# Performance work log

Measured on AMD Instinct MI355X. Metric: run time of the kernel, lower is better.

The kernel has to match this reference:

```python
import jax, jax.numpy as jnp
import numpy as np

# module hyperparams (match init_kwargs)
C, K, S, RATIO, GC = 64, 7, 2, 2, 16
G = C // GC                      # 4 groups
KK = K * K                       # 49
NS = int(RATIO * S)              # 4
NN = NS * NS                     # 16
PAD = (K - 1) // 2               # 3
C1_IN = G * (2 * K * GC + KK)    # 1092
C1_OUT = G * NN * KK // 10       # 313
C2_OUT = G * NN * KK             # 3136
EPS = 1e-5


def _unfold(x, k, s, p):
    # torch.nn.Unfold: patches ordered (C, ki, kj) channel-major
    B, Cc, H, W = x.shape
    xp = jnp.pad(x, ((0, 0), (0, 0), (p, p), (p, p)))
    Ho = (H + 2 * p - k) // s + 1
    Wo = (W + 2 * p - k) // s + 1
    rows = jnp.arange(Ho)[:, None] * s + jnp.arange(k)[None, :]      # (Ho,k)
    cols = jnp.arange(Wo)[:, None] * s + jnp.arange(k)[None, :]      # (Wo,k)
    pat = xp[:, :, rows[:, :, None, None], cols[None, None, :, :]]   # (B,C,Ho,k,Wo,k)
    return pat.transpose(0, 1, 3, 5, 2, 4)                            # (B,C,k,k,Ho,Wo)


def setup_inputs() -> dict:
    key = jax.random.key(0)
    ks = jax.random.split(key, 5)
    x = jax.random.normal(ks[0], (8, C, 64, 64), dtype=jnp.float32)
    w1 = jax.random.normal(ks[1], (C1_OUT, C1_IN), dtype=jnp.float32) * 0.02
    gamma = jnp.ones((C1_OUT,), dtype=jnp.float32)   # BN weight (constant_init 1)
    beta = jnp.zeros((C1_OUT,), dtype=jnp.float32)   # BN bias
    w2 = jax.random.normal(ks[2], (C2_OUT, C1_OUT), dtype=jnp.float32) * 0.02
    b2 = jnp.zeros((C2_OUT,), dtype=jnp.float32)
    return {"x": x, "w1": w1, "gamma": gamma, "beta": beta, "w2": w2, "b2": b2}


def reference(x, w1, gamma, beta, w2, b2):
    B, _, H, W = x.shape
    pat = _unfold(x, K, S, PAD)                          # (B,C,K,K,Ho,Wo)
    Ho, Wo = pat.shape[-2], pat.shape[-1]
    xg = pat.reshape(B, G, GC, K, K, Ho, Wo)
    # three axis-wise max pools -> per-pixel descriptor
    x1 = xg.max(axis=2).reshape(B, G * K * K, Ho, Wo)
    x2 = xg.max(axis=3).reshape(B, G * GC * K, Ho, Wo)
    x3 = xg.max(axis=4).reshape(B, G * GC * K, Ho, Wo)
    feat = jnp.concatenate([x1, x2, x3], axis=1)         # (B, C1_IN, Ho, Wo)
    # conv1: 1x1 conv (no bias) + BN (batch stats) + ReLU
    h = jnp.einsum('bchw,oc->bohw', feat, w1)
    mu = h.mean(axis=(0, 2, 3), keepdims=True)
    var = h.var(axis=(0, 2, 3), keepdims=True)
    h = gamma[None, :, None, None] * (h - mu) * jax.lax.rsqrt(var + EPS) + beta[None, :, None, None]
    h = jax.nn.relu(h)
    # conv2: 1x1 conv with bias
    h2 = jnp.einsum('bchw,oc->bohw', h, w2) + b2[None, :, None, None]
    wt = h2.reshape(B, G, KK, NN, Ho, Wo)
    wt = jax.nn.softmax(wt, axis=2)                      # softmax over kernel positions
    # softmax-weighted patch reduction (mean over k*k)
    xk = xg.reshape(B, G, GC, KK, Ho, Wo)
    out = jnp.einsum('bgckhw,bgknhw->bgcnhw', xk, wt) / KK
    out = out.reshape(B, C, NS, NS, Ho, Wo)
    out = out.transpose(0, 1, 4, 2, 5, 3).reshape(B, C, Ho * NS, Wo * NS)
    return out
```

## Files before the change

### kernel.cpp

```cpp
#include <hip/hip_runtime.h>

namespace {
constexpr int kB    = 8;
constexpr int kC    = 64;
constexpr int kH    = 64, kW = 64;
constexpr int kNP   = 8192;
constexpr int kC1In = 1092;
constexpr int kKP   = 1152;
constexpr int kC1Out= 313;
constexpr int kC2Out= 3136;
constexpr int kC1P  = 320;
constexpr int kRowS = 56;
constexpr int kPosS = 16 * kRowS + 8;
}

typedef __attribute__((ext_vector_type(8))) short bf16x8;
typedef __attribute__((ext_vector_type(8))) _Float16 f16x8;
typedef __attribute__((ext_vector_type(2))) _Float16 h16x2;
typedef __attribute__((ext_vector_type(4))) float f32x4;

__device__ __forceinline__ unsigned short f2bf(float f) {
    unsigned u = __float_as_uint(f);
    unsigned r = (u + 0x7fffu + ((u >> 16) & 1u)) >> 16;
    return (unsigned short)r;
}

__global__ void k_w2split(const float* __restrict__ w2, bf16x8* __restrict__ w2t) {
    int idx = blockIdx.x * 256 + threadIdx.x;
    int lane = idx & 63;
    int t = (idx >> 6) % 10;
    int k = (idx / 640) % 49;
    int g = idx / 31360;
    int n = lane & 15, c0 = t * 32 + ((lane >> 4) << 3);
    int row = g * 784 + k * 16 + n;
    bf16x8 hi;
    #pragma unroll
    for (int e = 0; e < 8; ++e) {
        int c = c0 + e;
        float v = (c < kC1Out) ? w2[(size_t)row * kC1Out + c] : 0.f;
        hi[e] = (short)f2bf(v);
    }
    w2t[idx] = hi;
}

__global__ void k_w1cvt(const float* __restrict__ w1, unsigned short* __restrict__ w1s) {
    int idx = blockIdx.x * 256 + threadIdx.x;
    if (idx >= kC1P * kKP) return;
    int r = idx / kKP, c = idx - r * kKP;
    float v = (r < kC1Out && c < kC1In) ? w1[(size_t)r * kC1In + c] : 0.f;
    w1s[idx] = f2bf(v);
}

__global__ __launch_bounds__(256) void k_feat(const float* __restrict__ x,
                                              unsigned short* __restrict__ feat_bf) {
    __shared__ float xs[16 * 7 * 40];
    int tid = threadIdx.x;
    int g = blockIdx.x, pt = blockIdx.y;
    int p0 = pt * 16;
    int b = p0 >> 10, i = (p0 >> 5) & 31, j0 = p0 & 31;
    int y0 = 2 * i - 3, xbase = 2 * j0 - 3;
    const float* xb = x + ((size_t)(b * 64 + g * 16) << 12);

    for (int idx = tid; idx < 16 * 7 * 40; idx += 256) {
        int ch = idx / 280, r2 = idx - ch * 280;
        int row = r2 / 40, col = r2 - row * 40;
        int yy = y0 + row, xx = xbase + col;
        float v = 0.f;
        if ((unsigned)yy < 64u && (unsigned)xx < 64u)
            v = xb[(ch << 12) + (yy << 6) + xx];
        xs[idx] = v;
    }
    __syncthreads();

    for (int o = tid; o < 16 * 273; o += 256) {
        int pos = o / 273, c = o - pos * 273;
        float m = -INFINITY;
        int cg;
        if (c < 49) {
            int a = c / 7, bk = c - a * 7;
            int base = a * 40 + 2 * pos + bk;
            #pragma unroll
            for (int ch = 0; ch < 16; ++ch) m = fmaxf(m, xs[ch * 280 + base]);
            cg = g * 49 + c;
        } else if (c < 161) {
            int r = c - 49;
            int ch = r / 7, bk = r - ch * 7;
            int base = ch * 280 + 2 * pos + bk;
            #pragma unroll
            for (int a = 0; a < 7; ++a) m = fmaxf(m, xs[base + a * 40]);
            cg = 196 + g * 112 + r;
        } else {
            int r = c - 161;
            int ch = r / 7, a = r - ch * 7;
            int base = ch * 280 + a * 40 + 2 * pos;
            #pragma unroll
            for (int bk = 0; bk < 7; ++bk) m = fmaxf(m, xs[base + bk]);
            cg = 644 + g * 112 + r;
        }
        feat_bf[(size_t)(p0 + pos) * kKP + cg] = f2bf(m);
    }
    if (g == 3) {
        for (int idx = tid; idx < 16 * 60; idx += 256) {
            int pos = idx / 60, c = idx - pos * 60;
            feat_bf[(size_t)(p0 + pos) * kKP + 1092 + c] = 0;
        }
    }
}

__global__ __launch_bounds__(256) void k_gemm1(
        const unsigned short* __restrict__ feat_bf, const unsigned short* __restrict__ w1s,
        float* __restrict__ h, float* __restrict__ sum_, float* __restrict__ sumsq_) {
    __shared__ unsigned short Ald[64 * 64];
    __shared__ unsigned short Bld[64 * 64];
    __shared__ float lsum[64], lsq[64];
    int tid = threadIdx.x;
    int lane = tid & 63, wv = tid >> 6;
    int row0 = blockIdx.x * 64, col0 = blockIdx.y * 64;
    int wr = wv >> 1, wc = wv & 1;
    int srow = lane >> 3;
    int soct = (lane & 7) ^ srow;
    int frow = lane & 15, fk = lane >> 4;

    f32x4 acc[2][2] = {};
    for (int k0 = 0; k0 < kKP; k0 += 64) {
        #pragma unroll
        for (int qq = 0; qq < 4; ++qq) {
            int q = wv + qq * 4;
            const unsigned short* srcbase;
            unsigned short* dst;
            int grow;
            if (q < 8) { grow = row0 + q * 8 + srow; srcbase = feat_bf; dst = Ald + q * 512; }
            else       { grow = col0 + (q - 8) * 8 + srow; srcbase = w1s; dst = Bld + (q - 8) * 512; }
            const unsigned short* src = srcbase + (size_t)grow * kKP + k0 + soct * 8;
            __builtin_amdgcn_global_load_lds(
                (const __attribute__((address_space(1))) unsigned int*)src,
                (__attribute__((address_space(3))) unsigned int*)dst, 16, 0, 0);
        }
        __syncthreads();
        #pragma unroll
        for (int ks = 0; ks < 2; ++ks) {
            int oct = ks * 4 + fk;
            bf16x8 a0, a1, b0, b1;
            { int r = wr * 32 + frow;      a0 = *(const bf16x8*)(Ald + (r * 8 + (oct ^ (r & 7))) * 8); }
            { int r = wr * 32 + 16 + frow; a1 = *(const bf16x8*)(Ald + (r * 8 + (oct ^ (r & 7))) * 8); }
            { int r = wc * 32 + frow;      b0 = *(const bf16x8*)(Bld + (r * 8 + (oct ^ (r & 7))) * 8); }
            { int r = wc * 32 + 16 + frow; b1 = *(const bf16x8*)(Bld + (r * 8 + (oct ^ (r & 7))) * 8); }
            acc[0][0] = __builtin_amdgcn_mfma_f32_16x16x32_bf16(a0, b0, acc[0][0], 0, 0, 0);
            acc[0][1] = __builtin_amdgcn_mfma_f32_16x16x32_bf16(a0, b1, acc[0][1], 0, 0, 0);
            acc[1][0] = __builtin_amdgcn_mfma_f32_16x16x32_bf16(a1, b0, acc[1][0], 0, 0, 0);
            acc[1][1] = __builtin_amdgcn_mfma_f32_16x16x32_bf16(a1, b1, acc[1][1], 0, 0, 0);
        }
        __syncthreads();
    }

    if (tid < 64) { lsum[tid] = 0.f; lsq[tid] = 0.f; }
    __syncthreads();
    #pragma unroll
    for (int i = 0; i < 2; ++i) {
        int mrow = row0 + wr * 32 + i * 16 + (lane >> 4) * 4;
        #pragma unroll
        for (int j = 0; j < 2; ++j) {
            int col_l = wc * 32 + j * 16 + (lane & 15);
            float s = 0.f, sq = 0.f;
            #pragma unroll
            for (int r = 0; r < 4; ++r) {
                float v = acc[i][j][r];
                h[(size_t)(mrow + r) * kC1P + col0 + col_l] = v;
                s += v; sq += v * v;
            }
            atomicAdd(&lsum[col_l], s);
            atomicAdd(&lsq[col_l], sq);
        }
    }
    __syncthreads();
    if (tid < 64 && col0 + tid < kC1Out) {
        atomicAdd(&sum_[col0 + tid], lsum[tid]);
        atomicAdd(&sumsq_[col0 + tid], lsq[tid]);
    }
}

__global__ void k_finalize(const float* __restrict__ sum_, const float* __restrict__ sumsq_,
                           const float* __restrict__ gamma, const float* __restrict__ beta,
                           float* __restrict__ scale, float* __restrict__ shift) {
    int o = blockIdx.x * 256 + threadIdx.x;
    if (o >= kC1Out) return;
    float mu  = sum_[o]   * (1.f / kNP);
    float var = sumsq_[o] * (1.f / kNP) - mu * mu;
    float sc  = gamma[o] * rsqrtf(var + 1e-5f);
    scale[o] = sc;
    shift[o] = beta[o] - mu * sc;
}

__global__ void k_split_h(const float* __restrict__ h,
                          const float* __restrict__ scale, const float* __restrict__ shift,
                          bf16x8* __restrict__ ht_hi) {
    int idx = blockIdx.x * 256 + threadIdx.x;
    int lane = idx & 63;
    int t = (idx >> 6) % 10;
    int ptile = idx / 640;
    int pos = ptile * 16 + (lane & 15);
    int c0 = t * 32 + ((lane >> 4) << 3);
    float vv[8];
    *(float4*)&vv[0] = *(const float4*)(h + (size_t)pos * kC1P + c0);
    *(float4*)&vv[4] = *(const float4*)(h + (size_t)pos * kC1P + c0 + 4);
    bf16x8 hi;
    #pragma unroll
    for (int e = 0; e < 8; ++e) {
        int c = c0 + e;
        float v = (c < kC1Out) ? fmaxf(vv[e] * scale[c] + shift[c], 0.f) : 0.f;
        hi[e] = (short)f2bf(v);
    }
    ht_hi[idx] = hi;
}

__global__ __launch_bounds__(512) void k_fused(
        const bf16x8* __restrict__ ht_hi, const bf16x8* __restrict__ w2t,
        const float* __restrict__ b2, const float* __restrict__ x,
        float* __restrict__ out) {
    __shared__ _Float16 wtb[32 * kPosS];
    __shared__ float invt[512];
    int tid = threadIdx.x;
    int lane = tid & 63, wv = tid >> 6;
    int bid = blockIdx.x;
    int g = bid >> 8, pt = bid & 255;

    bf16x8 a0[10], a1[10];
    {
        const bf16x8* hb = ht_hi + (size_t)(pt * 2) * 640 + lane;
        #pragma unroll
        for (int t = 0; t < 10; ++t) { a0[t] = hb[t * 64]; a1[t] = hb[640 + t * 64]; }
    }

    int col = lane & 15, rgrp = lane >> 4;
    for (int k = wv; k < 49; k += 8) {
        f32x4 acc0 = {0.f, 0.f, 0.f, 0.f};
        f32x4 acc1 = {0.f, 0.f, 0.f, 0.f};
        const bf16x8* wb = w2t + ((size_t)(g * 49 + k) * 10) * 64 + lane;
        #pragma unroll
        for (int t = 0; t < 10; ++t) {
            bf16x8 bh = wb[t * 64];
            acc0 = __builtin_amdgcn_mfma_f32_16x16x32_bf16(a0[t], bh, acc0, 0, 0, 0);
            acc1 = __builtin_amdgcn_mfma_f32_16x16x32_bf16(a1[t], bh, acc1, 0, 0, 0);
        }
        float bias = b2[g * 784 + k * 16 + col];
        #pragma unroll
        for (int r = 0; r < 4; ++r) {
            int pos = rgrp * 4 + r;
            wtb[pos * kPosS + col * kRowS + k]        = (_Float16)(acc0[r] + bias);
            wtb[(pos + 16) * kPosS + col * kRowS + k] = (_Float16)(acc1[r] + bias);
        }
    }
    __syncthreads();

    {
        int pos = tid >> 4, n = tid & 15;
        _Float16* base = wtb + pos * kPosS + n * kRowS;
        f16x8 row[7];
        #pragma unroll
        for (int c = 0; c < 7; ++c) row[c] = *(const f16x8*)(base + c * 8);
        float m = -INFINITY;
        #pragma unroll
        for (int c = 0; c < 7; ++c)
            #pragma unroll
            for (int e = 0; e < 8; ++e)
                if (c * 8 + e < 49) m = fmaxf(m, (float)row[c][e]);
        float s = 0.f;
        #pragma unroll
        for (int c = 0; c < 7; ++c) {
            f16x8 ee;
            #pragma unroll
            for (int e = 0; e < 8; ++e) {
                if (c * 8 + e < 49) {
                    float ex = __expf((float)row[c][e] - m);
                    s += ex;
                    ee[e] = (_Float16)ex;
                } else ee[e] = (_Float16)0.f;
            }
            *(f16x8*)(base + c * 8) = ee;
        }
        invt[tid] = 1.f / (s * 49.f);
    }
    __syncthreads();

    {
        int pos = tid & 31, c16 = tid >> 5;
        int p = pt * 32 + pos;
        int b = p >> 10, i = (p >> 5) & 31, j = p & 31;
        int y0 = 2 * i - 3, x0c = 2 * j - 3;
        const float* xc = x + (((size_t)b * 64 + g * 16 + c16) << 12);
        h16x2 patch2[28];
        #pragma unroll
        for (int a = 0; a < 7; ++a) {
            int yy = y0 + a;
            #pragma unroll
            for (int bk = 0; bk < 7; ++bk) {
                int kk = a * 7 + bk, xx = x0c + bk;
                float v = ((unsigned)yy < 64u && (unsigned)xx < 64u)
                        ? xc[(yy << 6) + xx] : 0.f;
                patch2[kk >> 1][kk & 1] = (_Float16)v;
            }
        }
        patch2[24][1] = (_Float16)0.f;
        patch2[25] = (h16x2)(_Float16)0.f;
        patch2[26] = (h16x2)(_Float16)0.f;
        patch2[27] = (h16x2)(_Float16)0.f;

        const _Float16* prow = wtb + pos * kPosS;
        float* outb = out + (((size_t)b * 64 + g * 16 + c16) << 14);
        #pragma unroll
        for (int n1 = 0; n1 < 4; ++n1) {
            f32x4 st;
            #pragma unroll
            for (int n2 = 0; n2 < 4; ++n2) {
                int n = n1 * 4 + n2;
                const f16x8* row = (const f16x8*)(prow + n * kRowS);
                float acc = 0.f;
                #pragma unroll
                for (int c = 0; c < 7; ++c) {
                    f16x8 w = row[c];
                    #pragma unroll
                    for (int q = 0; q < 4; ++q) {
                        h16x2 wp; wp[0] = w[2 * q]; wp[1] = w[2 * q + 1];
                        acc = __builtin_amdgcn_fdot2(patch2[c * 4 + q], wp, acc, false);
                    }
                }
                st[n2] = acc * invt[pos * 16 + n];
            }
            *(f32x4*)(outb + (i * 4 + n1) * 128 + j * 4) = st;
        }
    }
}

extern "C" void kernel_launch(void* const* d_in, const int* in_sizes, int n_in,
                              void* d_out, int out_size, void* d_ws, size_t ws_size,
                              hipStream_t stream) {
    const float* x     = (const float*)d_in[0];
    const float* w1    = (const float*)d_in[1];
    const float* gamma = (const float*)d_in[2];
    const float* beta  = (const float*)d_in[3];
    const float* w2    = (const float*)d_in[4];
    const float* b2    = (const float*)d_in[5];
    float* out = (float*)d_out;

    float* ws = (float*)d_ws;
    unsigned short* feat_bf = (unsigned short*)ws;
    float* h       = ws + 4718592;
    float* w2t_f   = h + 2621440;
    unsigned short* w1s = (unsigned short*)(w2t_f + 501760);
    float* sum_   = w2t_f + 501760 + 184320;
    float* sumsq_ = sum_ + 320;
    float* scale  = sumsq_ + 320;
    float* shift  = scale + 320;

    bf16x8* ht_hi = (bf16x8*)ws;
    bf16x8* w2t   = (bf16x8*)w2t_f;

    hipMemsetAsync(sum_, 0, 2 * 320 * sizeof(float), stream);
    k_w2split<<<490, 256, 0, stream>>>(w2, w2t);
    k_w1cvt<<<(kC1P * kKP + 255) / 256, 256, 0, stream>>>(w1, w1s);
    k_feat<<<dim3(4, 512), 256, 0, stream>>>(x, feat_bf);
    k_gemm1<<<dim3(kNP / 64, 5), 256, 0, stream>>>(feat_bf, w1s, h, sum_, sumsq_);
    k_finalize<<<2, 256, 0, stream>>>(sum_, sumsq_, gamma, beta, scale, shift);
    k_split_h<<<1280, 256, 0, stream>>>(h, scale, shift, ht_hi);
    k_fused<<<1024, 512, 0, stream>>>(ht_hi, w2t, b2, x, out);
}
```

Measured before the change: 129.8 us.

## Enlarge gemm1 row tile, transpose softmax staging layout, fold stats memset

The first GEMM now uses 128-row tiles with 512 threads (8 waves), so each loaded w1 tile is reused across twice as many feature rows and the grid shrinks. In the fused kernel, conv2 results are written k-major (stride 16) to avoid LDS bank conflicts on the scattered writes; softmax reads them strided, then after a barrier writes exponentials back in the original row layout. The BN statistics memset is folded into the w1 conversion kernel, removing one API call. The gemm1 epilogue (wr/wc mapping with 8 waves) is not shown being updated, so its correctness is uncertain.

```diff
diff --git a/kernel.cpp b/kernel.cpp
--- a/kernel.cpp
+++ b/kernel.cpp
@@ -43,8 +43,10 @@
     w2t[idx] = hi;
 }
 
-__global__ void k_w1cvt(const float* __restrict__ w1, unsigned short* __restrict__ w1s) {
+__global__ void k_w1cvt(const float* __restrict__ w1, unsigned short* __restrict__ w1s,
+                        float* __restrict__ stats) {
     int idx = blockIdx.x * 256 + threadIdx.x;
+    if (idx < 640) stats[idx] = 0.f;
     if (idx >= kC1P * kKP) return;
     int r = idx / kKP, c = idx - r * kKP;
     float v = (r < kC1Out && c < kC1In) ? w1[(size_t)r * kC1In + c] : 0.f;
@@ -107,15 +109,15 @@
     }
 }
 
-__global__ __launch_bounds__(256) void k_gemm1(
+__global__ __launch_bounds__(512) void k_gemm1(
         const unsigned short* __restrict__ feat_bf, const unsigned short* __restrict__ w1s,
         float* __restrict__ h, float* __restrict__ sum_, float* __restrict__ sumsq_) {
-    __shared__ unsigned short Ald[64 * 64];
+    __shared__ unsigned short Ald[128 * 64];
     __shared__ unsigned short Bld[64 * 64];
     __shared__ float lsum[64], lsq[64];
     int tid = threadIdx.x;
     int lane = tid & 63, wv = tid >> 6;
-    int row0 = blockIdx.x * 64, col0 = blockIdx.y * 64;
+    int row0 = blockIdx.x * 128, col0 = blockIdx.y * 64;
     int wr = wv >> 1, wc = wv & 1;
     int srow = lane >> 3;
     int soct = (lane & 7) ^ srow;
@@ -124,13 +126,13 @@
     f32x4 acc[2][2] = {};
     for (int k0 = 0; k0 < kKP; k0 += 64) {
         #pragma unroll
-        for (int qq = 0; qq < 4; ++qq) {
-            int q = wv + qq * 4;
+        for (int qq = 0; qq < 3; ++qq) {
+            int q = wv + qq * 8;
             const unsigned short* srcbase;
             unsigned short* dst;
             int grow;
-            if (q < 8) { grow = row0 + q * 8 + srow; srcbase = feat_bf; dst = Ald + q * 512; }
-            else       { grow = col0 + (q - 8) * 8 + srow; srcbase = w1s; dst = Bld + (q - 8) * 512; }
+            if (q < 16) { grow = row0 + q * 8 + srow; srcbase = feat_bf; dst = Ald + q * 512; }
+            else        { grow = col0 + (q - 16) * 8 + srow; srcbase = w1s; dst = Bld + (q - 16) * 512; }
             const unsigned short* src = srcbase + (size_t)grow * kKP + k0 + soct * 8;
             __builtin_amdgcn_global_load_lds(
                 (const __attribute__((address_space(1))) unsigned int*)src,
@@ -246,38 +248,44 @@
         #pragma unroll
         for (int r = 0; r < 4; ++r) {
             int pos = rgrp * 4 + r;
-            wtb[pos * kPosS + col * kRowS + k]        = (_Float16)(acc0[r] + bias);
-            wtb[(pos + 16) * kPosS + col * kRowS + k] = (_Float16)(acc1[r] + bias);
+            wtb[pos * kPosS + k * 16 + col]        = (_Float16)(acc0[r] + bias);
+            wtb[(pos + 16) * kPosS + k * 16 + col] = (_Float16)(acc1[r] + bias);
         }
     }
     __syncthreads();
 
     {
         int pos = tid >> 4, n = tid & 15;
-        _Float16* base = wtb + pos * kPosS + n * kRowS;
-        f16x8 row[7];
-        #pragma unroll
-        for (int c = 0; c < 7; ++c) row[c] = *(const f16x8*)(base + c * 8);
+        const _Float16* baseA = wtb + pos * kPosS + n;
+        f16x8 ee[7];
         float m = -INFINITY;
         #pragma unroll
         for (int c = 0; c < 7; ++c)
             #pragma unroll
-            for (int e = 0; e < 8; ++e)
-                if (c * 8 + e < 49) m = fmaxf(m, (float)row[c][e]);
+            for (int e = 0; e < 8; ++e) {
+                int k = c * 8 + e;
+                if (k < 49) {
+                    _Float16 v = baseA[k * 16];
+                    ee[c][e] = v;
+                    m = fmaxf(m, (float)v);
+                } else ee[c][e] = (_Float16)0.f;
+            }
         float s = 0.f;
         #pragma unroll
-        for (int c = 0; c < 7; ++c) {
-            f16x8 ee;
+        for (int c = 0; c < 7; ++c)
             #pragma unroll
             for (int e = 0; e < 8; ++e) {
-                if (c * 8 + e < 49) {
-                    float ex = __expf((float)row[c][e] - m);
+                int k = c * 8 + e;
+                if (k < 49) {
+                    float ex = __expf((float)ee[c][e] - m);
                     s += ex;
-                    ee[e] = (_Float16)ex;
-                } else ee[e] = (_Float16)0.f;
-            }
-            *(f16x8*)(base + c * 8) = ee;
-        }
+                    ee[c][e] = (_Float16)ex;
+                }
+            }
+        __syncthreads();
+        _Float16* baseB = wtb + pos * kPosS + n * kRowS;
+        #pragma unroll
+        for (int c = 0; c < 7; ++c) *(f16x8*)(baseB + c * 8) = ee[c];
         invt[tid] = 1.f / (s * 49.f);
     }
     __syncthreads();
@@ -355,11 +363,10 @@
     bf16x8* ht_hi = (bf16x8*)ws;
     bf16x8* w2t   = (bf16x8*)w2t_f;
 
-    hipMemsetAsync(sum_, 0, 2 * 320 * sizeof(float), stream);
     k_w2split<<<490, 256, 0, stream>>>(w2, w2t);
-    k_w1cvt<<<(kC1P * kKP + 255) / 256, 256, 0, stream>>>(w1, w1s);
+    k_w1cvt<<<(kC1P * kKP + 255) / 256, 256, 0, stream>>>(w1, w1s, sum_);
     k_feat<<<dim3(4, 512), 256, 0, stream>>>(x, feat_bf);
-    k_gemm1<<<dim3(kNP / 64, 5), 256, 0, stream>>>(feat_bf, w1s, h, sum_, sumsq_);
+    k_gemm1<<<dim3(kNP / 128, 5), 512, 0, stream>>>(feat_bf, w1s, h, sum_, sumsq_);
     k_finalize<<<2, 256, 0, stream>>>(sum_, sumsq_, gamma, beta, scale, shift);
     k_split_h<<<1280, 256, 0, stream>>>(h, scale, shift, ht_hi);
     k_fused<<<1024, 512, 0, stream>>>(ht_hi, w2t, b2, x, out);
```

Measured after the change: 128.7 us. No clear change (-0.8%).
